# Optimization experiments

Measured on AMD Instinct MI355X. Metric: run time of the kernel, lower is better.

Reference implementation:

```python
import jax, jax.numpy as jnp
import numpy as np

S, B, TD = 1024, 2, 138
D, H, Dh, L, F = 1024, 16, 64, 8, 2048
EPS = 1e-5


def setup_inputs() -> dict:
    key = jax.random.key(0)
    ks = jax.random.split(key, 32)
    std = 0.02

    def w(k, shape):
        return (jax.random.normal(k, shape, jnp.float32) * std)

    return {
        'tokens': jax.random.normal(ks[0], (S, B, TD), jnp.float32),
        'Win': w(ks[1], (D, TD)), 'bin_': jnp.zeros((D,), jnp.float32),
        'pos_emb': w(ks[2], (S, D)),
        'Wq': w(ks[3], (L, D, D)), 'bq': jnp.zeros((L, D), jnp.float32),
        'Wk': w(ks[4], (L, D, D)), 'bk': jnp.zeros((L, D), jnp.float32),
        'Wv': w(ks[5], (L, D, D)), 'bv': jnp.zeros((L, D), jnp.float32),
        'Wo': w(ks[6], (L, D, D)), 'bo': jnp.zeros((L, D), jnp.float32),
        'W1': w(ks[7], (L, F, D)), 'b1': jnp.zeros((L, F), jnp.float32),
        'W2': w(ks[8], (L, D, F)), 'b2': jnp.zeros((L, D), jnp.float32),
        'g1': jnp.ones((L, D), jnp.float32), 'be1': jnp.zeros((L, D), jnp.float32),
        'g2': jnp.ones((L, D), jnp.float32), 'be2': jnp.zeros((L, D), jnp.float32),
        'Wh': w(ks[9], (1, D)), 'bh': jnp.zeros((1,), jnp.float32),
    }


def _ln(x, g, b):
    mu = jnp.mean(x, axis=-1, keepdims=True)
    var = jnp.mean(jnp.square(x - mu), axis=-1, keepdims=True)
    return (x - mu) * jax.lax.rsqrt(var + EPS) * g + b


def _rope_tables(seq_len):
    inv_freq = 1.0 / (10000.0 ** (jnp.arange(0, Dh, 2, dtype=jnp.float32) / Dh))
    ang = jnp.arange(seq_len, dtype=jnp.float32)[:, None] * inv_freq  # (S, Dh/2)
    cos = jnp.repeat(jnp.cos(ang), 2, axis=-1)  # (S, Dh) interleaved
    sin = jnp.repeat(jnp.sin(ang), 2, axis=-1)
    return cos, sin


def _apply_rope(x, cos, sin):
    # x: (B, H, S, Dh); rotate_every_two: pairs (x0, x1) -> (-x1, x0)
    rot = jnp.stack([-x[..., 1::2], x[..., 0::2]], axis=-1).reshape(x.shape)
    return x * cos + rot * sin


def reference(tokens, Win, bin_, pos_emb, Wq, bq, Wk, bk, Wv, bv, Wo, bo,
              W1, b1, W2, b2, g1, be1, g2, be2, Wh, bh):
    s = tokens.shape[0]
    x = jnp.einsum('sbt,dt->sbd', tokens, Win) + bin_ + pos_emb[:s, None, :]
    cos, sin = _rope_tables(s)
    causal = jnp.tril(jnp.ones((s, s), dtype=bool))
    scale = 1.0 / np.sqrt(Dh)

    def to_heads(y):  # (S,B,D) -> (B,H,S,Dh)
        return jnp.transpose(y.reshape(s, -1, H, Dh), (1, 2, 0, 3))

    def layer(x, p):
        wq, bq_, wk, bk_, wv, bv_, wo, bo_, w1, b1_, w2, b2_, g1_, be1_, g2_, be2_ = p
        qh = _apply_rope(to_heads(jnp.einsum('sbd,ed->sbe', x, wq) + bq_), cos, sin)
        kh = _apply_rope(to_heads(jnp.einsum('sbd,ed->sbe', x, wk) + bk_), cos, sin)
        vh = to_heads(jnp.einsum('sbd,ed->sbe', x, wv) + bv_)
        scores = jnp.einsum('bhqd,bhkd->bhqk', qh, kh) * scale
        scores = jnp.where(causal, scores, -jnp.inf)
        attn = jax.nn.softmax(scores, axis=-1)
        o = jnp.einsum('bhqk,bhkd->bhqd', attn, vh)  # (B,H,S,Dh)
        o = jnp.transpose(o, (2, 0, 1, 3)).reshape(s, -1, D)
        attn_out = jnp.einsum('sbd,ed->sbe', o, wo) + bo_
        src2 = _ln(x + attn_out, g1_, be1_)
        ff = jnp.einsum('sbf,df->sbd', jax.nn.relu(jnp.einsum('sbd,fd->sbf', src2, w1) + b1_), w2) + b2_
        return _ln(src2 + ff, g2_, be2_), None

    params = (Wq, bq, Wk, bk, Wv, bv, Wo, bo, W1, b1, W2, b2, g1, be1, g2, be2)
    x, _ = jax.lax.scan(layer, x, params)
    return jnp.einsum('sbd,od->sbo', x, Wh) + bh  # (S, B, 1)
```

## Files before the change

### kernel.cpp

```cpp
#include <hip/hip_runtime.h>
#include <hip/hip_bf16.h>

typedef __hip_bfloat16 bf16;
typedef float f32x4 __attribute__((ext_vector_type(4)));
typedef float f32x16 __attribute__((ext_vector_type(16)));
typedef short s16x8 __attribute__((ext_vector_type(8)));
typedef int i32x4 __attribute__((ext_vector_type(4)));

#define S_LEN 1024
#define BATCH 2
#define TDIM 138
#define KPAD 192
#define DMOD 1024
#define NHEAD 16
#define DHEAD 64
#define NLAYER 8
#define FDIM 2048
#define MROWS 2048
static const size_t DD_ = (size_t)DMOD * DMOD;
static const size_t FD_ = (size_t)FDIM * DMOD;
static const size_t LW_ = 4 * DD_ + 2 * FD_;

__device__ __forceinline__ void load_lds16(const bf16* g, bf16* l) {
  __builtin_amdgcn_global_load_lds((const __attribute__((address_space(1))) void*)g,
                                   (__attribute__((address_space(3))) void*)l, 16, 0, 0);
}

__device__ __forceinline__ unsigned pack2(float a, float b) {
  unsigned x = __builtin_bit_cast(unsigned short, __float2bfloat16(a));
  unsigned y = __builtin_bit_cast(unsigned short, __float2bfloat16(b));
  return x | (y << 16);
}

__device__ __forceinline__ int chunk_start(int c) {
  return c == 0 ? 0 : (c == 1 ? 32 : (c == 2 ? 56 : 72));
}

__global__ __launch_bounds__(256) void f2b_all(
    const float4* __restrict__ Wq, const float4* __restrict__ Wk,
    const float4* __restrict__ Wv, const float4* __restrict__ Wo,
    const float4* __restrict__ W1, const float4* __restrict__ W2,
    ushort4* __restrict__ dst, int nlay) {
  const int DD4 = (int)(DD_ / 4), FD4 = (int)(FD_ / 4), LW4 = 4 * DD4 + 2 * FD4;
  int total = nlay * LW4;
  for (int i = blockIdx.x * 256 + threadIdx.x; i < total; i += gridDim.x * 256) {
    int l = i / LW4, off = i - l * LW4;
    const float4* src; int o2;
    if (off < 3 * DD4) {
      int w = off / DD4; o2 = off - w * DD4 + l * DD4;
      src = w == 0 ? Wq : (w == 1 ? Wk : Wv);
    } else if (off < 4 * DD4) { src = Wo; o2 = off - 3 * DD4 + l * DD4; }
    else if (off < 4 * DD4 + FD4) { src = W1; o2 = off - 4 * DD4 + l * FD4; }
    else { src = W2; o2 = off - 4 * DD4 - FD4 + l * FD4; }
    float4 v = src[o2];
    ushort4 o;
    o.x = __builtin_bit_cast(unsigned short, __float2bfloat16(v.x));
    o.y = __builtin_bit_cast(unsigned short, __float2bfloat16(v.y));
    o.z = __builtin_bit_cast(unsigned short, __float2bfloat16(v.z));
    o.w = __builtin_bit_cast(unsigned short, __float2bfloat16(v.w));
    dst[i] = o;
  }
}

__global__ __launch_bounds__(256) void pad_cvt(const float* __restrict__ in,
                                               bf16* __restrict__ out, int R) {
  int i = blockIdx.x * 256 + threadIdx.x;
  if (i >= R * KPAD) return;
  int r = i / KPAD, t = i - r * KPAD;
  out[i] = __float2bfloat16(t < TDIM ? in[r * TDIM + t] : 0.0f);
}

__global__ __launch_bounds__(256) void rope_table(float2* __restrict__ t) {
  int idx = blockIdx.x * 256 + threadIdx.x;
  if (idx >= S_LEN * 32) return;
  int s = idx >> 5, i = idx & 31;
  float freq = __expf(-(float)i * (2.0f / (float)DHEAD) * 9.210340371976184f);
  float sn, cs;
  sincosf((float)s * freq, &sn, &cs);
  t[idx] = make_float2(cs, sn);
}

template<int EPI, int SPLITK>
__global__ __launch_bounds__(256) void gemm64(
    const bf16* __restrict__ A, const bf16* __restrict__ W,
    const float* __restrict__ b0p, const float* __restrict__ b1p, const float* __restrict__ b2p,
    const float2* __restrict__ rope2, float* __restrict__ Cf,
    bf16* __restrict__ Cb0, bf16* __restrict__ Cb1, bf16* __restrict__ Cb2,
    int N, int K, int nby) {
  constexpr int ASZ = 64 * 64, BSZ = 128 * 64;
  __shared__ bf16 As[2 * ASZ];
  __shared__ bf16 Bs[2 * BSZ];
  int nwg = gridDim.x, bid = blockIdx.x;
  int wg = (bid & 7) * (nwg >> 3) + (bid >> 3);
  int nbx = N >> 7;
  int by = wg % nby, bx2 = wg / nby;
  int kh = 0, bx = bx2;
  if constexpr (SPLITK == 2) { bx = bx2 % nbx; kh = bx2 / nbx; }
  int bn = bx * 128, bm = by * 64;
  int Kh = K / SPLITK, koff = kh * Kh;
  int tid = threadIdx.x, lane = tid & 63, w = tid >> 6;
  int lo = lane & 15, hi = lane >> 4;
  int wr = (w >> 1) * 32, wc = (w & 1) * 64;
  f32x4 acc[2][4] = {};

  int srow = tid >> 3;
  int scol = (tid & 7) * 8;
  int scolsw = scol ^ ((srow & 7) << 3);
  const bf16* gA = A + (size_t)(bm + srow) * K + koff + scolsw;
  const bf16* gB = W + (size_t)(bn + srow) * K + koff + scolsw;
  bf16* lA = As + srow * 64 + scol;
  bf16* lB = Bs + srow * 64 + scol;

  auto STAGE = [&](int k0, int b) {
    load_lds16(gA + k0, lA + b * ASZ);
    load_lds16(gA + (size_t)32 * K + k0, lA + b * ASZ + 32 * 64);
    load_lds16(gB + k0, lB + b * BSZ);
    load_lds16(gB + (size_t)32 * K + k0, lB + b * BSZ + 32 * 64);
    load_lds16(gB + (size_t)64 * K + k0, lB + b * BSZ + 64 * 64);
    load_lds16(gB + (size_t)96 * K + k0, lB + b * BSZ + 96 * 64);
  };

  int nt = Kh / 64;
  STAGE(0, 0);
  __syncthreads();
  int cur = 0;
  int rsw = (lo & 7) << 3;
  for (int t = 0; t < nt; t++) {
    if (t + 1 < nt) STAGE((t + 1) * 64, cur ^ 1);
    const bf16* Ab = As + cur * ASZ;
    const bf16* Bb = Bs + cur * BSZ;
#pragma unroll
    for (int ks = 0; ks < 2; ks++) {
      int col = ((ks * 32 + hi * 8) ^ rsw);
      s16x8 af[2], bfr[4];
#pragma unroll
      for (int mi = 0; mi < 2; mi++) af[mi] = *(const s16x8*)(Ab + (wr + mi * 16 + lo) * 64 + col);
#pragma unroll
      for (int nj = 0; nj < 4; nj++) bfr[nj] = *(const s16x8*)(Bb + (wc + nj * 16 + lo) * 64 + col);
#pragma unroll
      for (int mi = 0; mi < 2; mi++)
#pragma unroll
        for (int nj = 0; nj < 4; nj++)
          acc[mi][nj] = __builtin_amdgcn_mfma_f32_16x16x32_bf16(af[mi], bfr[nj], acc[mi][nj], 0, 0, 0);
    }
    __syncthreads();
    cur ^= 1;
  }

#pragma unroll
  for (int mi = 0; mi < 2; mi++)
#pragma unroll
    for (int nj = 0; nj < 4; nj++)
#pragma unroll
      for (int r = 0; r < 4; r++) {
        int m = bm + wr + mi * 16 + hi * 4 + r;
        int n = bn + wc + nj * 16 + lo;
        float v = acc[mi][nj][r];
        if constexpr (EPI == 0) {
          int which = n >> 10;
          int d = n & 1023, h = d >> 6, dh = d & 63;
          int s = m >> 1, bb = m & 1;
          const float* bp = which == 0 ? b0p : (which == 1 ? b1p : b2p);
          v += bp[d];
          if (which < 2) {
            float pv = __shfl_xor(v, 1);
            float2 cn = rope2[s * 32 + (dh >> 1)];
            float o = (dh & 1) ? (v * cn.x + pv * cn.y) : (v * cn.x - pv * cn.y);
            bf16* dst = which == 0 ? Cb0 : Cb1;
            dst[(((size_t)(bb * NHEAD + h)) * S_LEN + s) * DHEAD + dh] = __float2bfloat16(o);
          } else {
            Cb2[(((size_t)(bb * NHEAD + h)) * DHEAD + dh) * S_LEN + s] = __float2bfloat16(v);
          }
        } else if constexpr (EPI == 1) {
          if (SPLITK == 1 || kh == 0) v += b0p[n];
          Cf[((size_t)kh * MROWS + m) * N + n] = v;
        } else if constexpr (EPI == 2) {
          Cb0[(size_t)m * N + n] = __float2bfloat16(fmaxf(v + b0p[n], 0.0f));
        } else {
          float v2 = v + b0p[n] + b1p[(size_t)(m >> 1) * DMOD + n];
          Cf[(size_t)m * N + n] = v2;
          Cb0[(size_t)m * N + n] = __float2bfloat16(v2);
        }
      }
}

__global__ __launch_bounds__(256) void flash_part(const bf16* __restrict__ Q,
    const bf16* __restrict__ K, const bf16* __restrict__ Vt,
    float* __restrict__ pO, float* __restrict__ pML) {
  int bid = blockIdx.x;
  int xcd = bid & 7, idx = bid >> 3;
  int bh = xcd * 4 + idx / 20;
  int w = threadIdx.x >> 6, lane = threadIdx.x & 63;
  int widx = (idx % 20) * 4 + w;
  int c = widx < 32 ? 0 : (widx < 56 ? 1 : (widx < 72 ? 2 : 3));
  int qt = widx - chunk_start(c) + 8 * c;
  int l31 = lane & 31, hi1 = lane >> 5;
  int q0 = qt * 32, kc0 = c * 256;
  int kend = min(kc0 + 256, q0 + 32);
  int nkt = (kend - kc0 + 31) >> 5;

  const size_t qkb = (size_t)bh * S_LEN * DHEAD;
  const bf16* qp = Q + qkb + (size_t)(q0 + l31) * DHEAD + hi1 * 8;
  s16x8 bq0 = *(const s16x8*)(qp);
  s16x8 bq1 = *(const s16x8*)(qp + 16);
  s16x8 bq2 = *(const s16x8*)(qp + 32);
  s16x8 bq3 = *(const s16x8*)(qp + 48);
  const bf16* kB = K + qkb;
  const bf16* vB = Vt + qkb;
  f32x16 accO0 = {}, accO1 = {};
  float mv = -INFINITY, lv = 0.0f;
  const float SC = 0.18033688011112042f;

  auto loadTile = [&](int kc, s16x8& k0, s16x8& k1, s16x8& k2, s16x8& k3,
                      s16x8& v0, s16x8& v1, s16x8& v2, s16x8& v3) {
    const bf16* kp = kB + (size_t)(kc + l31) * DHEAD + hi1 * 8;
    k0 = *(const s16x8*)(kp);
    k1 = *(const s16x8*)(kp + 16);
    k2 = *(const s16x8*)(kp + 32);
    k3 = *(const s16x8*)(kp + 48);
    const bf16* vp = vB + (size_t)l31 * S_LEN + kc + hi1 * 8;
    v0 = *(const s16x8*)(vp);
    v1 = *(const s16x8*)(vp + 16);
    v2 = *(const s16x8*)(vp + (size_t)32 * S_LEN);
    v3 = *(const s16x8*)(vp + (size_t)32 * S_LEN + 16);
  };

  auto computeTile = [&](int kc, s16x8 ka0, s16x8 ka1, s16x8 ka2, s16x8 ka3,
                         s16x8 va00, s16x8 va01, s16x8 va10, s16x8 va11) {
    f32x16 st = {};
    st = __builtin_amdgcn_mfma_f32_32x32x16_bf16(ka0, bq0, st, 0, 0, 0);
    st = __builtin_amdgcn_mfma_f32_32x32x16_bf16(ka1, bq1, st, 0, 0, 0);
    st = __builtin_amdgcn_mfma_f32_32x32x16_bf16(ka2, bq2, st, 0, 0, 0);
    st = __builtin_amdgcn_mfma_f32_32x32x16_bf16(ka3, bq3, st, 0, 0, 0);

    bool diag = (kc >= q0);
    float pmax = -INFINITY;
#pragma unroll
    for (int j = 0; j < 16; j++) {
      float s = st[j] * SC;
      if (diag) {
        int krow = kc + (j & 3) + 8 * (j >> 2) + 4 * hi1;
        if (krow > q0 + l31) s = -INFINITY;
      }
      st[j] = s;
      pmax = fmaxf(pmax, s);
    }
    pmax = fmaxf(pmax, __shfl_xor(pmax, 32));
    float mnew = fmaxf(mv, pmax);
    float fs = exp2f(mv - mnew);
    float sum = 0.0f;
#pragma unroll
    for (int j = 0; j < 16; j++) {
      float e = exp2f(st[j] - mnew);
      st[j] = e;
      sum += e;
    }
    sum += __shfl_xor(sum, 32);
    lv = lv * fs + sum;
    mv = mnew;
    accO0 = accO0 * fs;
    accO1 = accO1 * fs;

    unsigned w0 = pack2(st[0], st[1]),   w1 = pack2(st[2], st[3]);
    unsigned w2 = pack2(st[4], st[5]),   w3 = pack2(st[6], st[7]);
    unsigned w4 = pack2(st[8], st[9]),   w5 = pack2(st[10], st[11]);
    unsigned w6 = pack2(st[12], st[13]), w7 = pack2(st[14], st[15]);
    unsigned xw0 = (unsigned)__shfl_xor((int)w0, 32), xw1 = (unsigned)__shfl_xor((int)w1, 32);
    unsigned xw2 = (unsigned)__shfl_xor((int)w2, 32), xw3 = (unsigned)__shfl_xor((int)w3, 32);
    unsigned xw4 = (unsigned)__shfl_xor((int)w4, 32), xw5 = (unsigned)__shfl_xor((int)w5, 32);
    unsigned xw6 = (unsigned)__shfl_xor((int)w6, 32), xw7 = (unsigned)__shfl_xor((int)w7, 32);
    bool hb = (hi1 != 0);
    i32x4 f0, f1;
    f0.x = (int)(hb ? xw2 : w0); f0.y = (int)(hb ? xw3 : w1);
    f0.z = (int)(hb ? w2 : xw0); f0.w = (int)(hb ? w3 : xw1);
    f1.x = (int)(hb ? xw6 : w4); f1.y = (int)(hb ? xw7 : w5);
    f1.z = (int)(hb ? w6 : xw4); f1.w = (int)(hb ? w7 : xw5);
    s16x8 pf0 = __builtin_bit_cast(s16x8, f0);
    s16x8 pf1 = __builtin_bit_cast(s16x8, f1);
    accO0 = __builtin_amdgcn_mfma_f32_32x32x16_bf16(va00, pf0, accO0, 0, 0, 0);
    accO0 = __builtin_amdgcn_mfma_f32_32x32x16_bf16(va01, pf1, accO0, 0, 0, 0);
    accO1 = __builtin_amdgcn_mfma_f32_32x32x16_bf16(va10, pf0, accO1, 0, 0, 0);
    accO1 = __builtin_amdgcn_mfma_f32_32x32x16_bf16(va11, pf1, accO1, 0, 0, 0);
  };

  s16x8 A0, A1, A2, A3, A4, A5, A6, A7;
  s16x8 B0, B1, B2, B3, B4, B5, B6, B7;
  loadTile(kc0, A0, A1, A2, A3, A4, A5, A6, A7);
  for (int kt = 0; kt < nkt; kt += 2) {
    if (kt + 1 < nkt) loadTile(kc0 + (kt + 1) * 32, B0, B1, B2, B3, B4, B5, B6, B7);
    computeTile(kc0 + kt * 32, A0, A1, A2, A3, A4, A5, A6, A7);
    if (kt + 1 < nkt) {
      if (kt + 2 < nkt) loadTile(kc0 + (kt + 2) * 32, A0, A1, A2, A3, A4, A5, A6, A7);
      computeTile(kc0 + (kt + 1) * 32, B0, B1, B2, B3, B4, B5, B6, B7);
    }
  }

  int pbase = bh * 80 + widx;
  float* po = pO + (size_t)pbase * 2048 + l31 * 64 + 4 * hi1;
#pragma unroll
  for (int jj = 0; jj < 4; jj++) {
    f32x4 v0 = {accO0[4 * jj], accO0[4 * jj + 1], accO0[4 * jj + 2], accO0[4 * jj + 3]};
    f32x4 v1 = {accO1[4 * jj], accO1[4 * jj + 1], accO1[4 * jj + 2], accO1[4 * jj + 3]};
    *(f32x4*)(po + 8 * jj) = v0;
    *(f32x4*)(po + 32 + 8 * jj) = v1;
  }
  if (hi1 == 0) {
    pML[pbase * 64 + l31] = mv;
    pML[pbase * 64 + 32 + l31] = lv;
  }
}

__global__ __launch_bounds__(256) void flash_merge(const float* __restrict__ pO,
    const float* __restrict__ pML, bf16* __restrict__ O) {
  int bid = blockIdx.x;
  int xcd = bid & 7, idx = bid >> 3;
  int bh = xcd * 4 + idx / 32, qt = idx % 32;
  int b = bh >> 4, h = bh & 15;
  int nch = (qt >> 3) + 1;
  int t = threadIdx.x;
  int dh = t & 63, r0 = t >> 6;
  int ibase = bh * 80;
#pragma unroll
  for (int j = 0; j < 8; j++) {
    int row = j * 4 + r0;
    float ms = -INFINITY;
    for (int cc = 0; cc < nch; cc++) {
      int wi = chunk_start(cc) + qt - 8 * cc;
      ms = fmaxf(ms, pML[(ibase + wi) * 64 + row]);
    }
    float l = 0.0f, o = 0.0f;
    for (int cc = 0; cc < nch; cc++) {
      int wi = chunk_start(cc) + qt - 8 * cc;
      float wgt = exp2f(pML[(ibase + wi) * 64 + row] - ms);
      l += wgt * pML[(ibase + wi) * 64 + 32 + row];
      o += wgt * pO[(size_t)(ibase + wi) * 2048 + row * 64 + dh];
    }
    int q = qt * 32 + row;
    O[((size_t)q * BATCH + b) * DMOD + h * DHEAD + dh] = __float2bfloat16(o / l);
  }
}

__global__ __launch_bounds__(256) void ln_kernel(const float* __restrict__ a,
    const float* __restrict__ r0, const float* __restrict__ r1,
    const float* __restrict__ g, const float* __restrict__ be,
    float* __restrict__ outf, bf16* __restrict__ outb) {
  int m = blockIdx.x;
  int tid = threadIdx.x;
  float vals[4];
  float s1 = 0.f, s2 = 0.f;
  for (int j = 0; j < 4; j++) {
    int d = tid + j * 256;
    size_t i = (size_t)m * DMOD + d;
    float v = a[i] + r0[i] + r1[i];
    vals[j] = v; s1 += v; s2 += v * v;
  }
  __shared__ float red[8];
  for (int d = 1; d < 64; d <<= 1) { s1 += __shfl_xor(s1, d); s2 += __shfl_xor(s2, d); }
  int w = tid >> 6, lane = tid & 63;
  if (lane == 0) { red[w] = s1; red[4 + w] = s2; }
  __syncthreads();
  s1 = red[0] + red[1] + red[2] + red[3];
  s2 = red[4] + red[5] + red[6] + red[7];
  float mean = s1 * (1.0f / DMOD);
  float var = s2 * (1.0f / DMOD) - mean * mean;
  float rstd = rsqrtf(var + 1e-5f);
  for (int j = 0; j < 4; j++) {
    int d = tid + j * 256;
    float o = (vals[j] - mean) * rstd * g[d] + be[d];
    outf[(size_t)m * DMOD + d] = o;
    outb[(size_t)m * DMOD + d] = __float2bfloat16(o);
  }
}

__global__ __launch_bounds__(256) void head_kernel(const float* __restrict__ x,
    const float* __restrict__ Wh, const float* __restrict__ bh, float* __restrict__ out) {
  int m = blockIdx.x * 4 + (threadIdx.x >> 6);
  int lane = threadIdx.x & 63;
  float s = 0.f;
  for (int j = 0; j < 16; j++) {
    int d = lane + j * 64;
    s += x[(size_t)m * DMOD + d] * Wh[d];
  }
  for (int d = 1; d < 64; d <<= 1) s += __shfl_xor(s, d);
  if (lane == 0) out[m] = s + bh[0];
}

extern "C" void kernel_launch(void* const* d_in, const int* in_sizes, int n_in,
                              void* d_out, int out_size, void* d_ws, size_t ws_size,
                              hipStream_t stream) {
  (void)in_sizes; (void)n_in; (void)out_size;
  const float* tokens = (const float*)d_in[0];
  const float* Win    = (const float*)d_in[1];
  const float* binp   = (const float*)d_in[2];
  const float* pos    = (const float*)d_in[3];
  const float* Wq     = (const float*)d_in[4];
  const float* bq     = (const float*)d_in[5];
  const float* Wk     = (const float*)d_in[6];
  const float* bk     = (const float*)d_in[7];
  const float* Wv     = (const float*)d_in[8];
  const float* bv     = (const float*)d_in[9];
  const float* Wo     = (const float*)d_in[10];
  const float* bo     = (const float*)d_in[11];
  const float* W1     = (const float*)d_in[12];
  const float* b1     = (const float*)d_in[13];
  const float* W2     = (const float*)d_in[14];
  const float* b2     = (const float*)d_in[15];
  const float* g1     = (const float*)d_in[16];
  const float* be1    = (const float*)d_in[17];
  const float* g2     = (const float*)d_in[18];
  const float* be2    = (const float*)d_in[19];
  const float* Wh     = (const float*)d_in[20];
  const float* bhp    = (const float*)d_in[21];
  float* out = (float*)d_out;

  char* p = (char*)d_ws;
  auto alloc = [&](size_t bytes) { char* r = p; p += (bytes + 255) & ~(size_t)255; return r; };
  float* xf   = (float*)alloc((size_t)MROWS * DMOD * 4);
  bf16*  xb   = (bf16*) alloc((size_t)MROWS * DMOD * 2);
  float* x2f  = (float*)alloc((size_t)MROWS * DMOD * 4);
  bf16*  x2b  = (bf16*) alloc((size_t)MROWS * DMOD * 2);
  float* tmpf = (float*)alloc((size_t)2 * MROWS * DMOD * 4);
  bf16*  qb   = (bf16*) alloc((size_t)MROWS * DMOD * 2);
  bf16*  kb   = (bf16*) alloc((size_t)MROWS * DMOD * 2);
  bf16*  vt   = (bf16*) alloc((size_t)MROWS * DMOD * 2);
  bf16*  ob   = (bf16*) alloc((size_t)MROWS * DMOD * 2);
  bf16*  hb   = (bf16*) alloc((size_t)MROWS * FDIM * 2);
  bf16*  tokb = (bf16*) alloc((size_t)MROWS * KPAD * 2);
  bf16*  winb = (bf16*) alloc((size_t)DMOD * KPAD * 2);
  float2* rope2 = (float2*)alloc((size_t)S_LEN * 32 * 8);
  float* pO   = (float*)alloc((size_t)32 * 80 * 2048 * 4);
  float* pML  = (float*)alloc((size_t)32 * 80 * 64 * 4);

  size_t used = (size_t)(p - (char*)d_ws);
  bool big = (ws_size - used) >= (size_t)NLAYER * LW_ * 2 + 1024;
  int nlayConv = big ? NLAYER : 1;
  bf16* wb = (bf16*)alloc((size_t)nlayConv * LW_ * 2);

  rope_table<<<(S_LEN * 32 + 255) / 256, 256, 0, stream>>>(rope2);
  pad_cvt<<<(MROWS * KPAD + 255) / 256, 256, 0, stream>>>(tokens, tokb, MROWS);
  pad_cvt<<<(DMOD * KPAD + 255) / 256, 256, 0, stream>>>(Win, winb, DMOD);
  if (big)
    f2b_all<<<2048, 256, 0, stream>>>(
        (const float4*)Wq, (const float4*)Wk, (const float4*)Wv,
        (const float4*)Wo, (const float4*)W1, (const float4*)W2,
        (ushort4*)wb, NLAYER);

  gemm64<3, 1><<<256, 256, 0, stream>>>(
      tokb, winb, binp, pos, nullptr, nullptr,
      xf, xb, nullptr, nullptr, DMOD, KPAD, 32);

  for (int l = 0; l < NLAYER; l++) {
    if (!big)
      f2b_all<<<2048, 256, 0, stream>>>(
          (const float4*)(Wq + l * DD_), (const float4*)(Wk + l * DD_),
          (const float4*)(Wv + l * DD_), (const float4*)(Wo + l * DD_),
          (const float4*)(W1 + l * FD_), (const float4*)(W2 + l * FD_),
          (ushort4*)wb, 1);
    bf16* wbl = big ? wb + (size_t)l * LW_ : wb;

    gemm64<0, 1><<<768, 256, 0, stream>>>(
        xb, wbl, bq + l * DMOD, bk + l * DMOD, bv + l * DMOD, rope2,
        nullptr, qb, kb, vt, 3 * DMOD, DMOD, 32);

    flash_part<<<640, 256, 0, stream>>>(qb, kb, vt, pO, pML);
    flash_merge<<<1024, 256, 0, stream>>>(pO, pML, ob);

    gemm64<1, 2><<<512, 256, 0, stream>>>(
        ob, wbl + 3 * DD_, bo + l * DMOD, nullptr, nullptr, nullptr,
        tmpf, nullptr, nullptr, nullptr, DMOD, DMOD, 32);

    ln_kernel<<<MROWS, 256, 0, stream>>>(xf, tmpf, tmpf + (size_t)MROWS * DMOD,
                                         g1 + l * DMOD, be1 + l * DMOD, x2f, x2b);

    gemm64<2, 1><<<512, 256, 0, stream>>>(
        x2b, wbl + 4 * DD_, b1 + l * FDIM, nullptr, nullptr, nullptr,
        nullptr, hb, nullptr, nullptr, FDIM, DMOD, 32);

    gemm64<1, 2><<<512, 256, 0, stream>>>(
        hb, wbl + 4 * DD_ + FD_, b2 + l * DMOD, nullptr, nullptr, nullptr,
        tmpf, nullptr, nullptr, nullptr, DMOD, FDIM, 32);

    ln_kernel<<<MROWS, 256, 0, stream>>>(x2f, tmpf, tmpf + (size_t)MROWS * DMOD,
                                         g2 + l * DMOD, be2 + l * DMOD, xf, xb);
  }

  head_kernel<<<MROWS / 4, 256, 0, stream>>>(xf, Wh, bhp, out);
}
```

Before: 1.452 ms.

## Widen weight conversion, store flash partials in bf16, regroup GEMM tile mapping

The weight conversion kernel now handles 8 floats per thread and writes 16-byte bf16 vectors instead of 8-byte ones. Flash-attention partial outputs are stored as bf16 instead of fp32, halving the partial-output write and read traffic between flash_part and flash_merge. The GEMM block-to-tile mapping is changed so each XCD handles a block of column tiles, with row tiles grouped in runs of 8, to improve L2 reuse of A and W. The bf16 partials lose some precision before the merge, and the new mapping assumes the grid divides evenly into these groups.

```diff
diff --git a/kernel.cpp b/kernel.cpp
--- a/kernel.cpp
+++ b/kernel.cpp
@@ -6,6 +6,7 @@
 typedef float f32x16 __attribute__((ext_vector_type(16)));
 typedef short s16x8 __attribute__((ext_vector_type(8)));
 typedef int i32x4 __attribute__((ext_vector_type(4)));
+typedef unsigned u32x2 __attribute__((ext_vector_type(2)));
 
 #define S_LEN 1024
 #define BATCH 2
@@ -40,25 +41,23 @@
     const float4* __restrict__ Wq, const float4* __restrict__ Wk,
     const float4* __restrict__ Wv, const float4* __restrict__ Wo,
     const float4* __restrict__ W1, const float4* __restrict__ W2,
-    ushort4* __restrict__ dst, int nlay) {
-  const int DD4 = (int)(DD_ / 4), FD4 = (int)(FD_ / 4), LW4 = 4 * DD4 + 2 * FD4;
-  int total = nlay * LW4;
+    s16x8* __restrict__ dst, int nlay) {
+  const int DD8 = (int)(DD_ / 8), FD8 = (int)(FD_ / 8), LW8 = 4 * DD8 + 2 * FD8;
+  int total = nlay * LW8;
   for (int i = blockIdx.x * 256 + threadIdx.x; i < total; i += gridDim.x * 256) {
-    int l = i / LW4, off = i - l * LW4;
+    int l = i / LW8, off = i - l * LW8;
     const float4* src; int o2;
-    if (off < 3 * DD4) {
-      int w = off / DD4; o2 = off - w * DD4 + l * DD4;
+    if (off < 3 * DD8) {
+      int w = off / DD8; o2 = off - w * DD8 + l * DD8;
       src = w == 0 ? Wq : (w == 1 ? Wk : Wv);
-    } else if (off < 4 * DD4) { src = Wo; o2 = off - 3 * DD4 + l * DD4; }
-    else if (off < 4 * DD4 + FD4) { src = W1; o2 = off - 4 * DD4 + l * FD4; }
-    else { src = W2; o2 = off - 4 * DD4 - FD4 + l * FD4; }
-    float4 v = src[o2];
-    ushort4 o;
-    o.x = __builtin_bit_cast(unsigned short, __float2bfloat16(v.x));
-    o.y = __builtin_bit_cast(unsigned short, __float2bfloat16(v.y));
-    o.z = __builtin_bit_cast(unsigned short, __float2bfloat16(v.z));
-    o.w = __builtin_bit_cast(unsigned short, __float2bfloat16(v.w));
-    dst[i] = o;
+    } else if (off < 4 * DD8) { src = Wo; o2 = off - 3 * DD8 + l * DD8; }
+    else if (off < 4 * DD8 + FD8) { src = W1; o2 = off - 4 * DD8 + l * FD8; }
+    else { src = W2; o2 = off - 4 * DD8 - FD8 + l * FD8; }
+    float4 a = src[2 * o2], b = src[2 * o2 + 1];
+    union { s16x8 v; unsigned u[4]; } r;
+    r.u[0] = pack2(a.x, a.y); r.u[1] = pack2(a.z, a.w);
+    r.u[2] = pack2(b.x, b.y); r.u[3] = pack2(b.z, b.w);
+    dst[i] = r.v;
   }
 }
 
@@ -91,9 +90,15 @@
   __shared__ bf16 As[2 * ASZ];
   __shared__ bf16 Bs[2 * BSZ];
   int nwg = gridDim.x, bid = blockIdx.x;
-  int wg = (bid & 7) * (nwg >> 3) + (bid >> 3);
+  int x = bid & 7, c = bid >> 3;
+  int chunkSz = nwg >> 3;
+  int bxc = chunkSz / nby;
+  int per = 8 * bxc;
+  int grp = c / per, r0_ = c - grp * per;
+  int bxl = r0_ >> 3, byg = r0_ & 7;
+  int by = grp * 8 + byg;
+  int bx2 = x * bxc + bxl;
   int nbx = N >> 7;
-  int by = wg % nby, bx2 = wg / nby;
   int kh = 0, bx = bx2;
   if constexpr (SPLITK == 2) { bx = bx2 % nbx; kh = bx2 / nbx; }
   int bn = bx * 128, bm = by * 64;
@@ -186,7 +191,7 @@
 
 __global__ __launch_bounds__(256) void flash_part(const bf16* __restrict__ Q,
     const bf16* __restrict__ K, const bf16* __restrict__ Vt,
-    float* __restrict__ pO, float* __restrict__ pML) {
+    bf16* __restrict__ pO, float* __restrict__ pML) {
   int bid = blockIdx.x;
   int xcd = bid & 7, idx = bid >> 3;
   int bh = xcd * 4 + idx / 20;
@@ -296,13 +301,16 @@
   }
 
   int pbase = bh * 80 + widx;
-  float* po = pO + (size_t)pbase * 2048 + l31 * 64 + 4 * hi1;
+  bf16* po = pO + (size_t)pbase * 2048 + l31 * 64 + 4 * hi1;
 #pragma unroll
   for (int jj = 0; jj < 4; jj++) {
-    f32x4 v0 = {accO0[4 * jj], accO0[4 * jj + 1], accO0[4 * jj + 2], accO0[4 * jj + 3]};
-    f32x4 v1 = {accO1[4 * jj], accO1[4 * jj + 1], accO1[4 * jj + 2], accO1[4 * jj + 3]};
-    *(f32x4*)(po + 8 * jj) = v0;
-    *(f32x4*)(po + 32 + 8 * jj) = v1;
+    u32x2 v0, v1;
+    v0.x = pack2(accO0[4 * jj], accO0[4 * jj + 1]);
+    v0.y = pack2(accO0[4 * jj + 2], accO0[4 * jj + 3]);
+    v1.x = pack2(accO1[4 * jj], accO1[4 * jj + 1]);
+    v1.y = pack2(accO1[4 * jj + 2], accO1[4 * jj + 3]);
+    *(u32x2*)(po + 8 * jj) = v0;
+    *(u32x2*)(po + 32 + 8 * jj) = v1;
   }
   if (hi1 == 0) {
     pML[pbase * 64 + l31] = mv;
@@ -310,7 +318,7 @@
   }
 }
 
-__global__ __launch_bounds__(256) void flash_merge(const float* __restrict__ pO,
+__global__ __launch_bounds__(256) void flash_merge(const bf16* __restrict__ pO,
     const float* __restrict__ pML, bf16* __restrict__ O) {
   int bid = blockIdx.x;
   int xcd = bid & 7, idx = bid >> 3;
@@ -333,7 +341,7 @@
       int wi = chunk_start(cc) + qt - 8 * cc;
       float wgt = exp2f(pML[(ibase + wi) * 64 + row] - ms);
       l += wgt * pML[(ibase + wi) * 64 + 32 + row];
-      o += wgt * pO[(size_t)(ibase + wi) * 2048 + row * 64 + dh];
+      o += wgt * __bfloat162float(pO[(size_t)(ibase + wi) * 2048 + row * 64 + dh]);
     }
     int q = qt * 32 + row;
     O[((size_t)q * BATCH + b) * DMOD + h * DHEAD + dh] = __float2bfloat16(o / l);
@@ -428,7 +436,7 @@
   bf16*  tokb = (bf16*) alloc((size_t)MROWS * KPAD * 2);
   bf16*  winb = (bf16*) alloc((size_t)DMOD * KPAD * 2);
   float2* rope2 = (float2*)alloc((size_t)S_LEN * 32 * 8);
-  float* pO   = (float*)alloc((size_t)32 * 80 * 2048 * 4);
+  bf16*  pO   = (bf16*) alloc((size_t)32 * 80 * 2048 * 2);
   float* pML  = (float*)alloc((size_t)32 * 80 * 64 * 4);
 
   size_t used = (size_t)(p - (char*)d_ws);
@@ -443,7 +451,7 @@
     f2b_all<<<2048, 256, 0, stream>>>(
         (const float4*)Wq, (const float4*)Wk, (const float4*)Wv,
         (const float4*)Wo, (const float4*)W1, (const float4*)W2,
-        (ushort4*)wb, NLAYER);
+        (s16x8*)wb, NLAYER);
 
   gemm64<3, 1><<<256, 256, 0, stream>>>(
       tokb, winb, binp, pos, nullptr, nullptr,
@@ -455,7 +463,7 @@
           (const float4*)(Wq + l * DD_), (const float4*)(Wk + l * DD_),
           (const float4*)(Wv + l * DD_), (const float4*)(Wo + l * DD_),
           (const float4*)(W1 + l * FD_), (const float4*)(W2 + l * FD_),
-          (ushort4*)wb, 1);
+          (s16x8*)wb, 1);
     bf16* wbl = big ? wb + (size_t)l * LW_ : wb;
 
     gemm64<0, 1><<<768, 256, 0, stream>>>(
```

New measurement: 1.414 ms. 2.6% less time.
